# Kernel optimization log

Measured on AMD Instinct MI355X. Metric: run time of the kernel, lower is better.

Reference implementation:

```python
import jax, jax.numpy as jnp
import numpy as np


def sparse_conv3d(images, kernel, default_value, base_plane, dilations=(1, 1, 1)):
    """Sparse 3D conv over a per-pixel base-plane-aligned volume.

    images:     [B, H, W, D, C]  local depth slabs per pixel
    kernel:     [kh, kw, kd, C, F]
    base_plane: [B, H, W, 1] int  global depth offset of slab start per pixel
    Neighbor sample at pixel (h', w') and local depth d uses that neighbor's
    local index d + od + base_plane[h,w] - base_plane[h',w']; out-of-range
    (spatial or depth) samples are filled with default_value.
    """
    B, H, W, D, C = images.shape
    kh, kw, kd, _, F = kernel.shape
    d0, d1, d2 = dilations
    bp = base_plane[..., 0].astype(jnp.int32)  # [B,H,W]
    hs = jnp.arange(H)
    ws = jnp.arange(W)
    ds = jnp.arange(D)
    dv = jnp.asarray(default_value, images.dtype).reshape(())
    out = jnp.zeros((B, H, W, D, F), images.dtype)
    for i in range(kh):
        oh = (i - kh // 2) * d0
        h_idx = hs + oh
        valid_h = (h_idx >= 0) & (h_idx < H)
        h_c = jnp.clip(h_idx, 0, H - 1)
        for j in range(kw):
            ow = (j - kw // 2) * d1
            w_idx = ws + ow
            valid_w = (w_idx >= 0) & (w_idx < W)
            w_c = jnp.clip(w_idx, 0, W - 1)
            # gather shifted neighbor slabs and their base offsets
            img_n = images[:, h_c][:, :, w_c]      # [B,H,W,D,C]
            bp_n = bp[:, h_c][:, :, w_c]            # [B,H,W]
            rel = (bp - bp_n)[..., None]            # depth realignment [B,H,W,1]
            sp_valid = (valid_h[None, :, None, None] & valid_w[None, None, :, None])
            for k in range(kd):
                od = (k - kd // 2) * d2
                d_idx = ds[None, None, None, :] + od + rel  # [B,H,W,D]
                valid = sp_valid & (d_idx >= 0) & (d_idx < D)
                d_c = jnp.clip(d_idx, 0, D - 1)
                vals = jnp.take_along_axis(img_n, d_c[..., None], axis=3)  # [B,H,W,D,C]
                vals = jnp.where(valid[..., None], vals, dv)
                out = out + jnp.einsum('bhwdc,cf->bhwdf', vals, kernel[i, j, k])
    return out


def setup_inputs() -> dict:
    key = jax.random.key(0)
    k1, k2, k3 = jax.random.split(key, 3)
    B, H, W, D, C, F = 2, 96, 128, 32, 16, 16
    images = jax.random.normal(k1, (B, H, W, D, C), dtype=jnp.float32)
    base_plane = jax.random.randint(k2, (B, H, W, 1), 0, 8, dtype=jnp.int32)
    kernel = jax.random.normal(k3, (3, 3, 3, C, F), dtype=jnp.float32) * 0.05
    default_value = jnp.zeros((1,), dtype=jnp.float32)
    return {"images": images, "base_plane": base_plane, "kernel": kernel,
            "default_value": default_value}


def reference(images, base_plane, kernel, default_value):
    return sparse_conv3d(images, kernel, default_value[0], base_plane, dilations=(1, 1, 1))
```

## Files before the change

### kernel.cpp

```cpp
#include <hip/hip_runtime.h>

typedef __attribute__((ext_vector_type(8))) short short8;
typedef __attribute__((ext_vector_type(4))) short s16x4;
typedef __attribute__((ext_vector_type(4))) float f32x4;

#define NB_H 96
#define NB_W 128
#define NB_D 32
#define NB_C 16
#define NB_F 16
#define NPIX (2 * NB_H * NB_W)
#define KB2_U16 (14 * 512)
#define WS_NEED ((size_t)KB2_U16 * 2)
#define SLAB_STRIDE 1536
#define NSLAB 18
#define DV_OFF (NSLAB * SLAB_STRIDE)

static __device__ __forceinline__ unsigned short f2bf(float f) {
  unsigned int u = __builtin_bit_cast(unsigned int, f);
  unsigned int r = (u + 0x7fffu + ((u >> 16) & 1u)) >> 16;
  return (unsigned short)r;
}


__global__ __launch_bounds__(256) void sconv3d_wprep(
    const float* __restrict__ kern, unsigned short* __restrict__ kb2) {
  const int i = blockIdx.x * 256 + threadIdx.x;
  if (i >= KB2_U16) return;
  const int p = i >> 9;
  const int f = (i >> 5) & 15;
  const int k = i & 31;
  int lo, hi;
  if (p < 12) {
    const int q = p / 3, m = p % 3;
    lo = (m == 0) ? 6 * q : (m == 1) ? 6 * q + 3 : 6 * q + 2;
    hi = (m == 0) ? 6 * q + 1 : (m == 1) ? 6 * q + 4 : 6 * q + 5;
  } else if (p == 12) { lo = 24; hi = 25; }
  else { lo = 26; hi = -1; }
  const int t = (k < 16) ? lo : hi;
  const int c = k & 15;
  kb2[i] = (t >= 0) ? f2bf(kern[(t * 16 + c) * 16 + f]) : (unsigned short)0;
}

__global__ __launch_bounds__(256, 4) void sconv3d_fused(
    const float* __restrict__ img, const int* __restrict__ bp,
    const unsigned short* __restrict__ kb2, const float* __restrict__ dvp,
    float* __restrict__ out) {
  __shared__ unsigned short S[(NSLAB + 1) * SLAB_STRIDE / 2];
  char* Sb = (char*)S;
  const int tid = threadIdx.x;
  const int lane = tid & 63;
  const int r = lane & 15;
  const int grp = lane >> 4;
  const int vc = (grp & 1) * 16;
  const int halfbit = grp >> 1;
  const int rA = r + halfbit - 1;
  const int rX = r + 1;
  const int voff_dv = DV_OFF + vc;

  short8 bfrag[14];
#pragma unroll
  for (int p = 0; p < 14; ++p)
    bfrag[p] = *(const short8*)(kb2 + p * 512 + r * 32 + grp * 8);

  const int bid = (blockIdx.x & 7) * 768 + (blockIdx.x >> 3);
  const int b = bid / (NB_H * 32);
  const int rem = bid - b * (NB_H * 32);
  const int h = rem >> 5;
  const int wb = (rem & 31) * 4;

  const int t2 = tid & 127;
  const int srow = t2 >> 2;
  const int scq = (t2 & 3) * 4;
#pragma unroll
  for (int pass = 0; pass < 9; ++pass) {
    const int s = pass * 2 + (tid >> 7);
    const int dh = s / 6, col = s - 6 * dh;
    const int hh = min(max(h + dh - 1, 0), NB_H - 1);
    const int ww = min(max(wb + col - 1, 0), NB_W - 1);
    const int nidx = (b * NB_H + hh) * NB_W + ww;
    const float4 v = *(const float4*)(img + nidx * (NB_D * NB_C) + t2 * 4);
    s16x4 o;
    o[0] = (short)f2bf(v.x); o[1] = (short)f2bf(v.y);
    o[2] = (short)f2bf(v.z); o[3] = (short)f2bf(v.w);
    *(s16x4*)(Sb + s * SLAB_STRIDE + srow * 48 + scq * 2) = o;
  }
  const unsigned short dvb = f2bf(dvp[0]);
  if (tid < 16) S[DV_OFF / 2 + tid] = dvb;

  const int wid = __builtin_amdgcn_readfirstlane((int)(tid >> 6));
  const int w = wb + wid;
  const int pix = (b * NB_H + h) * NB_W + w;
  const int bpc = bp[pix];

#define CALCN(DI, DJ, SV, BASE, REL)                                    \
  {                                                                     \
    const int hh = h + (DI), ww = w + (DJ);                             \
    SV = (hh >= 0) & (hh < NB_H) & (ww >= 0) & (ww < NB_W);             \
    const int hc = min(max(hh, 0), NB_H - 1);                           \
    const int wc = min(max(ww, 0), NB_W - 1);                           \
    REL = bpc - bp[(b * NB_H + hc) * NB_W + wc];                        \
    BASE = (((DI) + 1) * 6 + wid + (DJ) + 1) * SLAB_STRIDE;             \
  }

  int sv0, ba0, re0, sv1, ba1, re1, sv2, ba2, re2, sv3, ba3, re3;
  int sv4, ba4, re4, sv5, ba5, re5, sv6, ba6, re6, sv7, ba7, re7;
  int sv8, ba8, re8;
  CALCN(-1, -1, sv0, ba0, re0);
  CALCN(-1, 0, sv1, ba1, re1);
  CALCN(-1, 1, sv2, ba2, re2);
  CALCN(0, -1, sv3, ba3, re3);
  CALCN(0, 0, sv4, ba4, re4);
  CALCN(0, 1, sv5, ba5, re5);
  CALCN(1, -1, sv6, ba6, re6);
  CALCN(1, 0, sv7, ba7, re7);
  CALCN(1, 1, sv8, ba8, re8);
#undef CALCN

  __syncthreads();

  f32x4 acc0 = {0.f, 0.f, 0.f, 0.f};
  f32x4 acc1 = {0.f, 0.f, 0.f, 0.f};

#define PAIR_UNIF(P, SV, BA, RE)                                        \
  {                                                                     \
    const int ds0 = rA + (RE);                                          \
    int vo0 = (BA) + ds0 * 48 + vc;                                     \
    vo0 = ((SV) && (unsigned)ds0 < NB_D) ? vo0 : voff_dv;               \
    const short8 a0 = *(const short8*)(Sb + vo0);                       \
    acc0 = __builtin_amdgcn_mfma_f32_16x16x32_bf16(a0, bfrag[P], acc0, 0, 0, 0); \
    const int ds1 = ds0 + 16;                                           \
    int vo1 = (BA) + ds1 * 48 + vc;                                     \
    vo1 = ((SV) && (unsigned)ds1 < NB_D) ? vo1 : voff_dv;               \
    const short8 a1 = *(const short8*)(Sb + vo1);                       \
    acc1 = __builtin_amdgcn_mfma_f32_16x16x32_bf16(a1, bfrag[P], acc1, 0, 0, 0); \
  }

#define PAIR_MIX(P, SVE, BAE, REE, SVO, BAO, REO)                       \
  {                                                                     \
    const int relS = halfbit ? (REO) : (REE);                           \
    const int baS = halfbit ? (BAO) : (BAE);                            \
    const int svS = halfbit ? (SVO) : (SVE);                            \
    const int ds0 = rX + relS;                                          \
    int vo0 = baS + ds0 * 48 + vc;                                      \
    vo0 = (svS && (unsigned)ds0 < NB_D) ? vo0 : voff_dv;                \
    const short8 a0 = *(const short8*)(Sb + vo0);                       \
    acc0 = __builtin_amdgcn_mfma_f32_16x16x32_bf16(a0, bfrag[P], acc0, 0, 0, 0); \
    const int ds1 = ds0 + 16;                                           \
    int vo1 = baS + ds1 * 48 + vc;                                      \
    vo1 = (svS && (unsigned)ds1 < NB_D) ? vo1 : voff_dv;                \
    const short8 a1 = *(const short8*)(Sb + vo1);                       \
    acc1 = __builtin_amdgcn_mfma_f32_16x16x32_bf16(a1, bfrag[P], acc1, 0, 0, 0); \
  }

  PAIR_UNIF(0, sv0, ba0, re0);
  PAIR_UNIF(1, sv1, ba1, re1);
  PAIR_MIX(2, sv0, ba0, re0, sv1, ba1, re1);
  PAIR_UNIF(3, sv2, ba2, re2);
  PAIR_UNIF(4, sv3, ba3, re3);
  PAIR_MIX(5, sv2, ba2, re2, sv3, ba3, re3);
  PAIR_UNIF(6, sv4, ba4, re4);
  PAIR_UNIF(7, sv5, ba5, re5);
  PAIR_MIX(8, sv4, ba4, re4, sv5, ba5, re5);
  PAIR_UNIF(9, sv6, ba6, re6);
  PAIR_UNIF(10, sv7, ba7, re7);
  PAIR_MIX(11, sv6, ba6, re6, sv7, ba7, re7);
  PAIR_UNIF(12, sv8, ba8, re8);
  PAIR_MIX(13, sv8, ba8, re8, 0, ba8, re8);

#undef PAIR_UNIF
#undef PAIR_MIX

  const int obase = pix * (NB_D * NB_F);
#pragma unroll
  for (int rr = 0; rr < 4; ++rr) {
    out[obase + (grp * 4 + rr) * NB_F + r] = acc0[rr];
    out[obase + (grp * 4 + rr + 16) * NB_F + r] = acc1[rr];
  }
}

__global__ __launch_bounds__(256) void sconv3d_mfma(
    const float* __restrict__ img, const int* __restrict__ bp,
    const float* __restrict__ kern, const float* __restrict__ dvp,
    float* __restrict__ out, int npix) {
  __shared__ unsigned short Kb[28 * 256];
  const int tid = threadIdx.x;
  for (int idx = tid; idx < 28 * 256; idx += 256) {
    unsigned short v = 0;
    if (idx < 27 * 256) v = f2bf(kern[idx]);
    Kb[idx] = v;
  }
  __syncthreads();

  const int lane = tid & 63;
  const int grp = lane >> 4;
  const int r = lane & 15;
  const int c0 = (grp & 1) * 8;
  const int half = grp >> 1;

  short8 bfrag[14];
#pragma unroll
  for (int p = 0; p < 14; ++p) {
#pragma unroll
    for (int j = 0; j < 8; ++j) {
      const int k = 8 * grp + j;
      const int t = 2 * p + (k >> 4);
      bfrag[p][j] = (short)Kb[t * 256 + (k & 15) * 16 + r];
    }
  }

  const int pix = blockIdx.x * 4 + (tid >> 6);
  if (pix >= npix) return;
  const int b = pix / (NB_H * NB_W);
  const int rem = pix - b * (NB_H * NB_W);
  const int h = rem >> 7;
  const int w = rem & (NB_W - 1);

  const float dv = dvp[0];
  const int bpc = bp[pix];

  f32x4 acc0 = {0.f, 0.f, 0.f, 0.f};
  f32x4 acc1 = {0.f, 0.f, 0.f, 0.f};

#pragma unroll
  for (int p = 0; p < 14; ++p) {
    const int t = 2 * p + half;
    const int n = t / 3;
    const int kd = t - 3 * n;
    const int i = n / 3;
    const int j = n - 3 * i;
    const int hh = h + i - 1;
    const int ww = w + j - 1;
    const bool sv =
        (t < 27) && (hh >= 0) && (hh < NB_H) && (ww >= 0) && (ww < NB_W);
    const int hc = min(max(hh, 0), NB_H - 1);
    const int wc = min(max(ww, 0), NB_W - 1);
    const int nidx = (b * NB_H + hc) * NB_W + wc;
    const int rel = bpc - bp[nidx];
    const int base = nidx * (NB_D * NB_C);
    const int dsh = (kd - 1) + rel;

    const int ds0 = r + dsh;
    short8 a0;
    {
      float va[8];
      if (sv && (ds0 >= 0) && (ds0 < NB_D)) {
        const float4* pp = (const float4*)(img + base + ds0 * NB_C + c0);
        const float4 x = pp[0];
        const float4 y = pp[1];
        va[0] = x.x; va[1] = x.y; va[2] = x.z; va[3] = x.w;
        va[4] = y.x; va[5] = y.y; va[6] = y.z; va[7] = y.w;
      } else {
#pragma unroll
        for (int q = 0; q < 8; ++q) va[q] = dv;
      }
#pragma unroll
      for (int q = 0; q < 8; ++q) a0[q] = (short)f2bf(va[q]);
    }
    acc0 = __builtin_amdgcn_mfma_f32_16x16x32_bf16(a0, bfrag[p], acc0, 0, 0, 0);

    const int ds1 = ds0 + 16;
    short8 a1;
    {
      float va[8];
      if (sv && (ds1 >= 0) && (ds1 < NB_D)) {
        const float4* pp = (const float4*)(img + base + ds1 * NB_C + c0);
        const float4 x = pp[0];
        const float4 y = pp[1];
        va[0] = x.x; va[1] = x.y; va[2] = x.z; va[3] = x.w;
        va[4] = y.x; va[5] = y.y; va[6] = y.z; va[7] = y.w;
      } else {
#pragma unroll
        for (int q = 0; q < 8; ++q) va[q] = dv;
      }
#pragma unroll
      for (int q = 0; q < 8; ++q) a1[q] = (short)f2bf(va[q]);
    }
    acc1 = __builtin_amdgcn_mfma_f32_16x16x32_bf16(a1, bfrag[p], acc1, 0, 0, 0);
  }

  const int obase = pix * (NB_D * NB_F);
#pragma unroll
  for (int rr = 0; rr < 4; ++rr) {
    out[obase + (grp * 4 + rr) * NB_F + r] = acc0[rr];
    out[obase + (grp * 4 + rr + 16) * NB_F + r] = acc1[rr];
  }
}

extern "C" void kernel_launch(void* const* d_in, const int* in_sizes, int n_in,
                              void* d_out, int out_size, void* d_ws, size_t ws_size,
                              hipStream_t stream) {
  const float* img = (const float*)d_in[0];
  const int* bp = (const int*)d_in[1];
  const float* kern = (const float*)d_in[2];
  const float* dvp = (const float*)d_in[3];
  float* out = (float*)d_out;

  if (ws_size >= WS_NEED) {
    unsigned short* kb2 = (unsigned short*)d_ws;
    sconv3d_wprep<<<28, 256, 0, stream>>>(kern, kb2);
    sconv3d_fused<<<NPIX / 4, 256, 0, stream>>>(img, bp, kb2, dvp, out);
  } else {
    sconv3d_mfma<<<NPIX / 4, 256, 0, stream>>>(img, bp, kern, dvp, out, NPIX);
  }
}
```

Before: 43.06 us.

## Tile 2x4 pixels per block to share halo slabs and stream weight fragments

The fused kernel now handles a 2x4 pixel tile with 512 threads instead of a 1x4 row. It stages 24 neighbour slabs, where the old layout staged 18 slabs for 4 pixels, so each block reloads fewer halo slabs per output pixel. The LDS row stride drops from 48 to 40 bytes to cut shared-memory footprint and change the bank mapping. Weight fragments are now read from global or L2 on every MFMA pair instead of being held in 14 short8 registers, and the weight-prep layout is reordered so those reads are contiguous. Dropping the held fragments lowers register pressure so the launch bound of 8 blocks can hold, at the cost of extra repeated global loads; the custom bf16 rounding is also replaced with the library __float2bfloat16 conversion.

```diff
diff --git a/kernel.cpp b/kernel.cpp
--- a/kernel.cpp
+++ b/kernel.cpp
@@ -1,4 +1,5 @@
 #include <hip/hip_runtime.h>
+#include <hip/hip_bf16.h>
 
 typedef __attribute__((ext_vector_type(8))) short short8;
 typedef __attribute__((ext_vector_type(4))) short s16x4;
@@ -12,14 +13,13 @@
 #define NPIX (2 * NB_H * NB_W)
 #define KB2_U16 (14 * 512)
 #define WS_NEED ((size_t)KB2_U16 * 2)
-#define SLAB_STRIDE 1536
-#define NSLAB 18
+#define SLAB_STRIDE 1280
+#define NSLAB 24
 #define DV_OFF (NSLAB * SLAB_STRIDE)
-
-static __device__ __forceinline__ unsigned short f2bf(float f) {
-  unsigned int u = __builtin_bit_cast(unsigned int, f);
-  unsigned int r = (u + 0x7fffu + ((u >> 16) & 1u)) >> 16;
-  return (unsigned short)r;
+#define LDS_U16 ((DV_OFF + 64) / 2)
+
+static __device__ __forceinline__ short fcvt(float f) {
+  return (short)__builtin_bit_cast(unsigned short, __float2bfloat16(f));
 }
 
 
@@ -28,8 +28,10 @@
   const int i = blockIdx.x * 256 + threadIdx.x;
   if (i >= KB2_U16) return;
   const int p = i >> 9;
-  const int f = (i >> 5) & 15;
-  const int k = i & 31;
+  const int g = (i >> 7) & 3;
+  const int f = (i >> 3) & 15;
+  const int j = i & 7;
+  const int k = g * 8 + j;
   int lo, hi;
   if (p < 12) {
     const int q = p / 3, m = p % 3;
@@ -39,14 +41,15 @@
   else { lo = 26; hi = -1; }
   const int t = (k < 16) ? lo : hi;
   const int c = k & 15;
-  kb2[i] = (t >= 0) ? f2bf(kern[(t * 16 + c) * 16 + f]) : (unsigned short)0;
-}
-
-__global__ __launch_bounds__(256, 4) void sconv3d_fused(
+  kb2[i] = (t >= 0) ? (unsigned short)fcvt(kern[(t * 16 + c) * 16 + f])
+                    : (unsigned short)0;
+}
+
+__global__ __launch_bounds__(512, 8) void sconv3d_fused2(
     const float* __restrict__ img, const int* __restrict__ bp,
     const unsigned short* __restrict__ kb2, const float* __restrict__ dvp,
     float* __restrict__ out) {
-  __shared__ unsigned short S[(NSLAB + 1) * SLAB_STRIDE / 2];
+  __shared__ unsigned short S[LDS_U16];
   char* Sb = (char*)S;
   const int tid = threadIdx.x;
   const int lane = tid & 63;
@@ -58,49 +61,44 @@
   const int rX = r + 1;
   const int voff_dv = DV_OFF + vc;
 
-  short8 bfrag[14];
-#pragma unroll
-  for (int p = 0; p < 14; ++p)
-    bfrag[p] = *(const short8*)(kb2 + p * 512 + r * 32 + grp * 8);
-
-  const int bid = (blockIdx.x & 7) * 768 + (blockIdx.x >> 3);
-  const int b = bid / (NB_H * 32);
-  const int rem = bid - b * (NB_H * 32);
-  const int h = rem >> 5;
-  const int wb = (rem & 31) * 4;
+  const int bid = (blockIdx.x & 7) * 384 + (blockIdx.x >> 3);
+  const int b = bid >= (48 * 32);
+  const int rem = bid - b * (48 * 32);
+  const int h0 = (rem >> 5) * 2;
+  const int w0 = (rem & 31) * 4;
 
   const int t2 = tid & 127;
+  const int sg = tid >> 7;
   const int srow = t2 >> 2;
-  const int scq = (t2 & 3) * 4;
-#pragma unroll
-  for (int pass = 0; pass < 9; ++pass) {
-    const int s = pass * 2 + (tid >> 7);
-    const int dh = s / 6, col = s - 6 * dh;
-    const int hh = min(max(h + dh - 1, 0), NB_H - 1);
-    const int ww = min(max(wb + col - 1, 0), NB_W - 1);
-    const int nidx = (b * NB_H + hh) * NB_W + ww;
-    const float4 v = *(const float4*)(img + nidx * (NB_D * NB_C) + t2 * 4);
+  const int sb8 = (t2 & 3) * 8;
+#pragma unroll
+  for (int pass = 0; pass < 6; ++pass) {
+    const int s = pass * 4 + sg;
+    const int dh = s / 6, dw = s - 6 * dh;
+    const int hh = min(max(h0 + dh - 1, 0), NB_H - 1);
+    const int ww = min(max(w0 + dw - 1, 0), NB_W - 1);
+    const float4 v = *(const float4*)(
+        img + ((b * NB_H + hh) * NB_W + ww) * (NB_D * NB_C) + t2 * 4);
     s16x4 o;
-    o[0] = (short)f2bf(v.x); o[1] = (short)f2bf(v.y);
-    o[2] = (short)f2bf(v.z); o[3] = (short)f2bf(v.w);
-    *(s16x4*)(Sb + s * SLAB_STRIDE + srow * 48 + scq * 2) = o;
-  }
-  const unsigned short dvb = f2bf(dvp[0]);
-  if (tid < 16) S[DV_OFF / 2 + tid] = dvb;
+    o[0] = fcvt(v.x); o[1] = fcvt(v.y); o[2] = fcvt(v.z); o[3] = fcvt(v.w);
+    *(s16x4*)(Sb + s * SLAB_STRIDE + srow * 40 + sb8) = o;
+  }
+  if (tid < 16) S[DV_OFF / 2 + tid] = (unsigned short)fcvt(dvp[0]);
 
   const int wid = __builtin_amdgcn_readfirstlane((int)(tid >> 6));
-  const int w = wb + wid;
+  const int ph = wid >> 2, pw = wid & 3;
+  const int h = h0 + ph, w = w0 + pw;
   const int pix = (b * NB_H + h) * NB_W + w;
   const int bpc = bp[pix];
 
-#define CALCN(DI, DJ, SV, BASE, REL)                                    \
+#define CALCN(DI, DJ, SV, BA, RE)                                       \
   {                                                                     \
     const int hh = h + (DI), ww = w + (DJ);                             \
     SV = (hh >= 0) & (hh < NB_H) & (ww >= 0) & (ww < NB_W);             \
     const int hc = min(max(hh, 0), NB_H - 1);                           \
     const int wc = min(max(ww, 0), NB_W - 1);                           \
-    REL = bpc - bp[(b * NB_H + hc) * NB_W + wc];                        \
-    BASE = (((DI) + 1) * 6 + wid + (DJ) + 1) * SLAB_STRIDE;             \
+    RE = bpc - bp[(b * NB_H + hc) * NB_W + wc];                         \
+    BA = ((ph + (DI) + 1) * 6 + pw + (DJ) + 1) * SLAB_STRIDE;           \
   }
 
   int sv0, ba0, re0, sv1, ba1, re1, sv2, ba2, re2, sv3, ba3, re3;
@@ -122,35 +120,39 @@
   f32x4 acc0 = {0.f, 0.f, 0.f, 0.f};
   f32x4 acc1 = {0.f, 0.f, 0.f, 0.f};
 
+#define BFRAG(P) (*(const short8*)(kb2 + (P) * 512 + grp * 128 + r * 8))
+
 #define PAIR_UNIF(P, SV, BA, RE)                                        \
   {                                                                     \
+    const short8 bf = BFRAG(P);                                         \
     const int ds0 = rA + (RE);                                          \
-    int vo0 = (BA) + ds0 * 48 + vc;                                     \
+    int vo0 = (BA) + ds0 * 40 + vc;                                     \
     vo0 = ((SV) && (unsigned)ds0 < NB_D) ? vo0 : voff_dv;               \
     const short8 a0 = *(const short8*)(Sb + vo0);                       \
-    acc0 = __builtin_amdgcn_mfma_f32_16x16x32_bf16(a0, bfrag[P], acc0, 0, 0, 0); \
+    acc0 = __builtin_amdgcn_mfma_f32_16x16x32_bf16(a0, bf, acc0, 0, 0, 0); \
     const int ds1 = ds0 + 16;                                           \
-    int vo1 = (BA) + ds1 * 48 + vc;                                     \
+    int vo1 = (BA) + ds1 * 40 + vc;                                     \
     vo1 = ((SV) && (unsigned)ds1 < NB_D) ? vo1 : voff_dv;               \
     const short8 a1 = *(const short8*)(Sb + vo1);                       \
-    acc1 = __builtin_amdgcn_mfma_f32_16x16x32_bf16(a1, bfrag[P], acc1, 0, 0, 0); \
+    acc1 = __builtin_amdgcn_mfma_f32_16x16x32_bf16(a1, bf, acc1, 0, 0, 0); \
   }
 
 #define PAIR_MIX(P, SVE, BAE, REE, SVO, BAO, REO)                       \
   {                                                                     \
+    const short8 bf = BFRAG(P);                                         \
     const int relS = halfbit ? (REO) : (REE);                           \
     const int baS = halfbit ? (BAO) : (BAE);                            \
     const int svS = halfbit ? (SVO) : (SVE);                            \
     const int ds0 = rX + relS;                                          \
-    int vo0 = baS + ds0 * 48 + vc;                                      \
+    int vo0 = baS + ds0 * 40 + vc;                                      \
     vo0 = (svS && (unsigned)ds0 < NB_D) ? vo0 : voff_dv;                \
     const short8 a0 = *(const short8*)(Sb + vo0);                       \
-    acc0 = __builtin_amdgcn_mfma_f32_16x16x32_bf16(a0, bfrag[P], acc0, 0, 0, 0); \
+    acc0 = __builtin_amdgcn_mfma_f32_16x16x32_bf16(a0, bf, acc0, 0, 0, 0); \
     const int ds1 = ds0 + 16;                                           \
-    int vo1 = baS + ds1 * 48 + vc;                                      \
+    int vo1 = baS + ds1 * 40 + vc;                                      \
     vo1 = (svS && (unsigned)ds1 < NB_D) ? vo1 : voff_dv;                \
     const short8 a1 = *(const short8*)(Sb + vo1);                       \
-    acc1 = __builtin_amdgcn_mfma_f32_16x16x32_bf16(a1, bfrag[P], acc1, 0, 0, 0); \
+    acc1 = __builtin_amdgcn_mfma_f32_16x16x32_bf16(a1, bf, acc1, 0, 0, 0); \
   }
 
   PAIR_UNIF(0, sv0, ba0, re0);
@@ -170,6 +172,7 @@
 
 #undef PAIR_UNIF
 #undef PAIR_MIX
+#undef BFRAG
 
   const int obase = pix * (NB_D * NB_F);
 #pragma unroll
@@ -187,7 +190,7 @@
   const int tid = threadIdx.x;
   for (int idx = tid; idx < 28 * 256; idx += 256) {
     unsigned short v = 0;
-    if (idx < 27 * 256) v = f2bf(kern[idx]);
+    if (idx < 27 * 256) v = (unsigned short)fcvt(kern[idx]);
     Kb[idx] = v;
   }
   __syncthreads();
@@ -255,7 +258,7 @@
         for (int q = 0; q < 8; ++q) va[q] = dv;
       }
 #pragma unroll
-      for (int q = 0; q < 8; ++q) a0[q] = (short)f2bf(va[q]);
+      for (int q = 0; q < 8; ++q) a0[q] = fcvt(va[q]);
     }
     acc0 = __builtin_amdgcn_mfma_f32_16x16x32_bf16(a0, bfrag[p], acc0, 0, 0, 0);
 
@@ -274,7 +277,7 @@
         for (int q = 0; q < 8; ++q) va[q] = dv;
       }
 #pragma unroll
-      for (int q = 0; q < 8; ++q) a1[q] = (short)f2bf(va[q]);
+      for (int q = 0; q < 8; ++q) a1[q] = fcvt(va[q]);
     }
     acc1 = __builtin_amdgcn_mfma_f32_16x16x32_bf16(a1, bfrag[p], acc1, 0, 0, 0);
   }
@@ -299,7 +302,7 @@
   if (ws_size >= WS_NEED) {
     unsigned short* kb2 = (unsigned short*)d_ws;
     sconv3d_wprep<<<28, 256, 0, stream>>>(kern, kb2);
-    sconv3d_fused<<<NPIX / 4, 256, 0, stream>>>(img, bp, kb2, dvp, out);
+    sconv3d_fused2<<<NPIX / 8, 512, 0, stream>>>(img, bp, kb2, dvp, out);
   } else {
     sconv3d_mfma<<<NPIX / 4, 256, 0, stream>>>(img, bp, kern, dvp, out, NPIX);
   }
```

After: 87.49 us. 103% more time.
